# Performance work log

Hardware: AMD Instinct MI355X
Metric: run time of the kernel (lower is better)

## Reference

```python
import jax, jax.numpy as jnp
import numpy as np

B, T, L, H = 512, 512, 64, 512  # batch, time_steps, sequence_len, hidden_dim


def gru_cell(x, h, W_ih, W_hh, b_ih, b_hh):
    # PyTorch GRUCell math. W_ih: [3H, in], W_hh: [3H, H]; gate order (r, z, n).
    gi = x @ W_ih.T + b_ih
    gh = h @ W_hh.T + b_hh
    i_r, i_z, i_n = jnp.split(gi, 3, axis=-1)
    h_r, h_z, h_n = jnp.split(gh, 3, axis=-1)
    r = jax.nn.sigmoid(i_r + h_r)
    z = jax.nn.sigmoid(i_z + h_z)
    n = jnp.tanh(i_n + r * h_n)
    return (1.0 - z) * n + z * h


def setup_inputs() -> dict:
    key = jax.random.key(0)
    ks = jax.random.split(key, 12)
    s = 1.0 / np.sqrt(H)  # PyTorch GRUCell/Linear init scale
    u = lambda k, shape: jax.random.uniform(k, shape, jnp.float32, -s, s)
    return {
        "x": jax.random.normal(ks[0], (B, T + L - 1), jnp.float32),
        "h_1": jnp.zeros((B, H), jnp.float32),
        "h_2": jnp.zeros((B, H), jnp.float32),
        "W_ih1": u(ks[1], (3 * H, T)),
        "W_hh1": u(ks[2], (3 * H, H)),
        "b_ih1": u(ks[3], (3 * H,)),
        "b_hh1": u(ks[4], (3 * H,)),
        "W_ih2": u(ks[5], (3 * H, H)),
        "W_hh2": u(ks[6], (3 * H, H)),
        "b_ih2": u(ks[7], (3 * H,)),
        "b_hh2": u(ks[8], (3 * H,)),
        "W_fc": u(ks[9], (1, H)),
        "b_fc": u(ks[10], (1,)),
    }


def reference(x, h_1, h_2, W_ih1, W_hh1, b_ih1, b_hh1,
              W_ih2, W_hh2, b_ih2, b_hh2, W_fc, b_fc):
    # Sliding windows x[:, t:t+T] for t in [0, L): gather once, scan over steps.
    idx = jnp.arange(L)[:, None] + jnp.arange(T)[None, :]  # [L, T]
    xs = jnp.transpose(x[:, idx], (1, 0, 2))  # [L, B, T]

    def step(carry, x_t):
        h1, h2 = carry
        h1 = gru_cell(x_t, h1, W_ih1, W_hh1, b_ih1, b_hh1)
        h2 = gru_cell(h1, h2, W_ih2, W_hh2, b_ih2, b_hh2)
        y = (h2 @ W_fc.T + b_fc)[:, 0]  # [B]
        return (h1, h2), y

    (h1, h2), ys = jax.lax.scan(step, (h_1, h_2), xs)
    return ys.T, h1, h2  # output_seq [B, L], final hidden states
```

## Files before the change

### kernel.cpp

```cpp
#include <hip/hip_runtime.h>
#include <hip/hip_bf16.h>
#include <math.h>

typedef __attribute__((ext_vector_type(8))) short short8;
typedef __attribute__((ext_vector_type(4))) float f32x4;
typedef unsigned short u16;
typedef unsigned int u32;

__device__ __forceinline__ u16 f2bf(float f) {
  union { float f; u32 u; } x; x.f = f;
  return (u16)((x.u + 0x7fffu + ((x.u >> 16) & 1u)) >> 16);
}
__device__ __forceinline__ float sigm(float v) {
  return __builtin_amdgcn_rcpf(1.0f + __expf(-v));
}
__device__ __forceinline__ float tanh_fast(float v) {
  return 1.0f - 2.0f * __builtin_amdgcn_rcpf(1.0f + __expf(2.0f * v));
}

#define MFMA __builtin_amdgcn_mfma_f32_16x16x32_bf16
#define HS 262144

#define LDG16_BODY(FL)                                        \
    "global_load_dwordx4 %0, %16, off " FL "\n\t"             \
    "global_load_dwordx4 %1, %16, off offset:64 " FL "\n\t"   \
    "global_load_dwordx4 %2, %16, off offset:128 " FL "\n\t"  \
    "global_load_dwordx4 %3, %16, off offset:192 " FL "\n\t"  \
    "global_load_dwordx4 %4, %16, off offset:256 " FL "\n\t"  \
    "global_load_dwordx4 %5, %16, off offset:320 " FL "\n\t"  \
    "global_load_dwordx4 %6, %16, off offset:384 " FL "\n\t"  \
    "global_load_dwordx4 %7, %16, off offset:448 " FL "\n\t"  \
    "global_load_dwordx4 %8, %16, off offset:512 " FL "\n\t"  \
    "global_load_dwordx4 %9, %16, off offset:576 " FL "\n\t"  \
    "global_load_dwordx4 %10, %16, off offset:640 " FL "\n\t" \
    "global_load_dwordx4 %11, %16, off offset:704 " FL "\n\t" \
    "global_load_dwordx4 %12, %16, off offset:768 " FL "\n\t" \
    "global_load_dwordx4 %13, %16, off offset:832 " FL "\n\t" \
    "global_load_dwordx4 %14, %16, off offset:896 " FL "\n\t" \
    "global_load_dwordx4 %15, %16, off offset:960 " FL
#define LDG16_OPS(a, base)                                                     \
    : "=&v"(a[0]), "=&v"(a[1]), "=&v"(a[2]), "=&v"(a[3]), "=&v"(a[4]),         \
      "=&v"(a[5]), "=&v"(a[6]), "=&v"(a[7]), "=&v"(a[8]), "=&v"(a[9]),         \
      "=&v"(a[10]), "=&v"(a[11]), "=&v"(a[12]), "=&v"(a[13]), "=&v"(a[14]),    \
      "=&v"(a[15])                                                             \
    : "v"(base) : "memory"

__device__ __forceinline__ void ldg16nw_sc0(short8 a[16], const u16* base) {
  asm volatile(LDG16_BODY("sc0") LDG16_OPS(a, base));
}
__device__ __forceinline__ void ldg16nw_sc01(short8 a[16], const u16* base) {
  asm volatile(LDG16_BODY("sc0 sc1") LDG16_OPS(a, base));
}
#define VMCNT16() do { asm volatile("s_waitcnt vmcnt(16)" ::: "memory"); \
                       __builtin_amdgcn_sched_barrier(0); } while (0)
#define VMCNT0()  do { asm volatile("s_waitcnt vmcnt(0)"  ::: "memory"); \
                       __builtin_amdgcn_sched_barrier(0); } while (0)

__device__ __forceinline__ void stg_sc01(u32* p, u32 v) {
  asm volatile("global_store_dword %0, %1, off sc0 sc1" :: "v"(p), "v"(v) : "memory");
}
__device__ __forceinline__ u32 ldflag(const u32* p) {
  u32 v;
  asm volatile("global_load_dword %0, %1, off sc0 sc1\n\t"
               "s_waitcnt vmcnt(0)" : "=v"(v) : "v"(p) : "memory");
  return v;
}

__device__ __forceinline__ u32 wait_ge(const u32* flags, u32 target, int lane) {
  const u32* p = flags + (lane & 31);
  u32 v;
  for (;;) {
    v = ldflag(p);
    if (__ballot(v >= target) == ~0ull) break;
    __builtin_amdgcn_s_sleep(1);
  }
  #pragma unroll
  for (int k = 16; k; k >>= 1) {
    u32 o = (u32)__shfl_xor((int)v, k);
    v = v < o ? v : o;
  }
  return v;
}

__global__ __launch_bounds__(256, 1) void gru_fused(
    const float* __restrict__ xin, const float* __restrict__ h1in, const float* __restrict__ h2in,
    const float* __restrict__ Wih1, const float* __restrict__ Whh1,
    const float* __restrict__ bih1, const float* __restrict__ bhh1,
    const float* __restrict__ Wih2, const float* __restrict__ Whh2,
    const float* __restrict__ bih2, const float* __restrict__ bhh2,
    const float* __restrict__ Wfc, const float* __restrict__ bfc,
    float* __restrict__ out, u16* __restrict__ wsb, unsigned* __restrict__ barc)
{
  const int bid   = blockIdx.x;
  const int rb    = bid & 3;
  const int layer = (bid >> 2) & 1;
  const int cbl   = bid >> 3;
  const int n0    = cbl * 16;
  const int wid   = bid >> 2;
  const int tid   = threadIdx.x;
  const int w     = tid >> 6;
  const int lane  = tid & 63;
  const int quad  = lane >> 4;
  const int m16   = lane & 15;

  u16* x0  = wsb;
  u16* x1  = x0 + 512 * 576;
  u16* h1r = x1 + 512 * 576;
  u16* h2r = h1r + 4 * HS;
  u16* h1m = h2r + 4 * HS;

  __shared__ short8 wlds[96 * 64];

  u32* f0    = (u32*)barc + rb * 32;
  u32* f1    = (u32*)barc + 128 + rb * 32;
  unsigned* cinit = barc + 512;

  const float* Wih = layer ? Wih2 : Wih1;
  const float* Whh = layer ? Whh2 : Whh1;
  const float* bih = layer ? bih2 : bih1;
  const float* bhh = layer ? bhh2 : bhh1;

  for (int i = wid * 256 + tid; i < 128 * 575; i += 64 * 256) {
    int r = i / 575, c = i - r * 575;
    int row = rb * 128 + r;
    u16 bv = f2bf(xin[row * 575 + c]);
    x0[row * 576 + c] = bv;
    if (c >= 1) x1[row * 576 + (c - 1)] = bv;
  }
  for (int i = wid * 256 + tid; i < 128 * 512; i += 64 * 256) {
    int r = i >> 9, c = i & 511;
    int row = rb * 128 + r;
    u16 h1v = f2bf(h1in[row * 512 + c]);
    h1r[3 * HS + row * 512 + c] = h1v;
    h2r[3 * HS + row * 512 + c] = f2bf(h2in[row * 512 + c]);
  }
  for (int i = tid; i < 96 * 64; i += 256) {
    int blk = i >> 6, l = i & 63;
    int s, gr;
    if (blk < 64) { s = blk & 31; gr = (blk >> 5) * 512; }
    else          { s = blk - 64; gr = 1024; }
    int n  = n0 + (l & 15);
    int k0 = s * 32 + (l >> 4) * 8;
    short8 pk;
    #pragma unroll
    for (int j = 0; j < 8; ++j) {
      int k = k0 + j;
      float v = (k < 512) ? Wih[(gr + n) * 512 + k] : Whh[(gr + n) * 512 + (k - 512)];
      pk[j] = (short)f2bf(v);
    }
    wlds[blk * 64 + l] = pk;
  }

  float hreg[2][4];
  const float* hin = layer ? h2in : h1in;
  #pragma unroll
  for (int rf = 0; rf < 2; ++rf)
    #pragma unroll
    for (int q = 0; q < 4; ++q)
      hreg[rf][q] = hin[(rb * 128 + (2 * w + rf) * 16 + quad * 4 + q) * 512 + n0 + m16];

  const int nn = n0 + m16;
  const float bias_r  = bih[nn] + bhh[nn];
  const float bias_z  = bih[512 + nn] + bhh[512 + nn];
  const float bias_in = bih[1024 + nn];
  const float bias_hn = bhh[1024 + nn];
  const float wfc  = Wfc[nn];
  const float bfcv = bfc[0];

  __syncthreads();
  if (tid == 0) {
    __builtin_amdgcn_fence(__ATOMIC_RELEASE, "agent");
    __hip_atomic_fetch_add(cinit, 1u, __ATOMIC_RELAXED, __HIP_MEMORY_SCOPE_AGENT);
    while (__hip_atomic_load(cinit, __ATOMIC_RELAXED, __HIP_MEMORY_SCOPE_AGENT) < 256u)
      __builtin_amdgcn_s_sleep(1);
    __builtin_amdgcn_fence(__ATOMIC_ACQUIRE, "agent");
  }
  __syncthreads();

  const int arow0 = rb * 128 + (2 * w) * 16 + m16;
  const int arow1 = arow0 + 16;

  if (layer == 0) {
    u32 c1min = 0;
    for (int u = 0; u < 64; ++u) {
      if (u >= 4 && c1min < (u32)(u - 3)) c1min = wait_ge(f1, (u32)(u - 3), lane);
      f32x4 acc[2][4] = {};
      {
        const int c = u & 1;
        const u16* xc = c ? x1 : x0;
        const u32* pa0 = (const u32*)(xc + (size_t)arow0 * 576 + (u - c) + quad * 8);
        const u32* pa1 = (const u32*)(xc + (size_t)arow1 * 576 + (u - c) + quad * 8);
        #pragma unroll
        for (int s = 0; s < 16; ++s) {
          union { short8 v; u32 u4[4]; } a0, a1;
          #pragma unroll
          for (int j = 0; j < 4; ++j) { a0.u4[j] = pa0[s * 16 + j]; a1.u4[j] = pa1[s * 16 + j]; }
          short8 br = wlds[(s)      * 64 + lane];
          short8 bz = wlds[(32 + s) * 64 + lane];
          short8 bi = wlds[(64 + s) * 64 + lane];
          acc[0][0] = MFMA(a0.v, br, acc[0][0], 0, 0, 0);
          acc[1][0] = MFMA(a1.v, br, acc[1][0], 0, 0, 0);
          acc[0][1] = MFMA(a0.v, bz, acc[0][1], 0, 0, 0);
          acc[1][1] = MFMA(a1.v, bz, acc[1][1], 0, 0, 0);
          acc[0][2] = MFMA(a0.v, bi, acc[0][2], 0, 0, 0);
          acc[1][2] = MFMA(a1.v, bi, acc[1][2], 0, 0, 0);
        }
      }
      if (u > 0) wait_ge(f0, (u32)u, lane); else VMCNT0();
      {
        short8 a0[16], a1[16];
        const u16* hb = h1r + (size_t)((u + 3) & 3) * HS + quad * 8;
        ldg16nw_sc0(a0, hb + (size_t)arow0 * 512);
        ldg16nw_sc0(a1, hb + (size_t)arow1 * 512);
        VMCNT16();
        #pragma unroll
        for (int s = 0; s < 16; ++s) {
          short8 br = wlds[(16 + s) * 64 + lane];
          short8 bz = wlds[(48 + s) * 64 + lane];
          short8 bh = wlds[(80 + s) * 64 + lane];
          acc[0][0] = MFMA(a0[s], br, acc[0][0], 0, 0, 0);
          acc[0][1] = MFMA(a0[s], bz, acc[0][1], 0, 0, 0);
          acc[0][3] = MFMA(a0[s], bh, acc[0][3], 0, 0, 0);
        }
        VMCNT0();
        #pragma unroll
        for (int s = 0; s < 16; ++s) {
          short8 br = wlds[(16 + s) * 64 + lane];
          short8 bz = wlds[(48 + s) * 64 + lane];
          short8 bh = wlds[(80 + s) * 64 + lane];
          acc[1][0] = MFMA(a1[s], br, acc[1][0], 0, 0, 0);
          acc[1][1] = MFMA(a1[s], bz, acc[1][1], 0, 0, 0);
          acc[1][3] = MFMA(a1[s], bh, acc[1][3], 0, 0, 0);
        }
      }
      {
        u32* hw32 = (u32*)(h1r + (size_t)(u & 3) * HS);
        u32* hm   = (u32*)(h1m + (size_t)(u & 3) * HS);
        #pragma unroll
        for (int rf = 0; rf < 2; ++rf)
          #pragma unroll
          for (int q = 0; q < 4; ++q) {
            float rg = sigm(acc[rf][0][q] + bias_r);
            float zg = sigm(acc[rf][1][q] + bias_z);
            float ng = tanh_fast(acc[rf][2][q] + bias_in + rg * (acc[rf][3][q] + bias_hn));
            float hv = (1.0f - zg) * ng + zg * hreg[rf][q];
            hreg[rf][q] = hv;
            int row = rb * 128 + (2 * w + rf) * 16 + quad * 4 + q;
            u16 b = f2bf(hv);
            int pb = __shfl_xor((int)(u32)b, 1);
            if (!(m16 & 1)) {
              u32 pr = (u32)b | ((u32)(u16)pb << 16);
              int pi = (row * 512 + nn) >> 1;
              hw32[pi] = pr;
              stg_sc01(&hm[pi], pr);
            }
          }
      }
      asm volatile("s_waitcnt vmcnt(0)" ::: "memory");
      __syncthreads();
      if (tid == 0) stg_sc01(&f0[cbl], (u32)(u + 1));
    }
  } else {
    for (int v = 0; v < 64; ++v) {
      f32x4 acc[2][4] = {};
      if (v > 0) wait_ge(f1, (u32)v, lane); else VMCNT0();
      {
        short8 a0[16], a1[16];
        const u16* hb = h2r + (size_t)((v + 3) & 3) * HS + quad * 8;
        ldg16nw_sc0(a0, hb + (size_t)arow0 * 512);
        ldg16nw_sc0(a1, hb + (size_t)arow1 * 512);
        VMCNT16();
        #pragma unroll
        for (int s = 0; s < 16; ++s) {
          short8 br = wlds[(16 + s) * 64 + lane];
          short8 bz = wlds[(48 + s) * 64 + lane];
          short8 bh = wlds[(80 + s) * 64 + lane];
          acc[0][0] = MFMA(a0[s], br, acc[0][0], 0, 0, 0);
          acc[0][1] = MFMA(a0[s], bz, acc[0][1], 0, 0, 0);
          acc[0][3] = MFMA(a0[s], bh, acc[0][3], 0, 0, 0);
        }
        VMCNT0();
        #pragma unroll
        for (int s = 0; s < 16; ++s) {
          short8 br = wlds[(16 + s) * 64 + lane];
          short8 bz = wlds[(48 + s) * 64 + lane];
          short8 bh = wlds[(80 + s) * 64 + lane];
          acc[1][0] = MFMA(a1[s], br, acc[1][0], 0, 0, 0);
          acc[1][1] = MFMA(a1[s], bz, acc[1][1], 0, 0, 0);
          acc[1][3] = MFMA(a1[s], bh, acc[1][3], 0, 0, 0);
        }
      }
      wait_ge(f0, (u32)(v + 1), lane);
      {
        short8 a0[16], a1[16];
        const u16* hb = h1m + (size_t)(v & 3) * HS + quad * 8;
        ldg16nw_sc01(a0, hb + (size_t)arow0 * 512);
        ldg16nw_sc01(a1, hb + (size_t)arow1 * 512);
        VMCNT16();
        #pragma unroll
        for (int s = 0; s < 16; ++s) {
          short8 br = wlds[(s)      * 64 + lane];
          short8 bz = wlds[(32 + s) * 64 + lane];
          short8 bi = wlds[(64 + s) * 64 + lane];
          acc[0][0] = MFMA(a0[s], br, acc[0][0], 0, 0, 0);
          acc[0][1] = MFMA(a0[s], bz, acc[0][1], 0, 0, 0);
          acc[0][2] = MFMA(a0[s], bi, acc[0][2], 0, 0, 0);
        }
        VMCNT0();
        #pragma unroll
        for (int s = 0; s < 16; ++s) {
          short8 br = wlds[(s)      * 64 + lane];
          short8 bz = wlds[(32 + s) * 64 + lane];
          short8 bi = wlds[(64 + s) * 64 + lane];
          acc[1][0] = MFMA(a1[s], br, acc[1][0], 0, 0, 0);
          acc[1][1] = MFMA(a1[s], bz, acc[1][1], 0, 0, 0);
          acc[1][2] = MFMA(a1[s], bi, acc[1][2], 0, 0, 0);
        }
      }
      {
        u32* hw32 = (u32*)(h2r + (size_t)(v & 3) * HS);
        #pragma unroll
        for (int rf = 0; rf < 2; ++rf)
          #pragma unroll
          for (int q = 0; q < 4; ++q) {
            float rg = sigm(acc[rf][0][q] + bias_r);
            float zg = sigm(acc[rf][1][q] + bias_z);
            float ng = tanh_fast(acc[rf][2][q] + bias_in + rg * (acc[rf][3][q] + bias_hn));
            float hv = (1.0f - zg) * ng + zg * hreg[rf][q];
            hreg[rf][q] = hv;
            int row = rb * 128 + (2 * w + rf) * 16 + quad * 4 + q;
            u16 b = f2bf(hv);
            int pb = __shfl_xor((int)(u32)b, 1);
            if (!(m16 & 1))
              hw32[(row * 512 + nn) >> 1] = (u32)b | ((u32)(u16)pb << 16);
          }
      }
      asm volatile("s_waitcnt vmcnt(0)" ::: "memory");
      __syncthreads();
      if (tid == 0) stg_sc01(&f1[cbl], (u32)(v + 1));
      #pragma unroll
      for (int rf = 0; rf < 2; ++rf)
        #pragma unroll
        for (int q = 0; q < 4; ++q) {
          float yv = hreg[rf][q] * wfc;
          yv += __shfl_xor(yv, 1);
          yv += __shfl_xor(yv, 2);
          yv += __shfl_xor(yv, 4);
          yv += __shfl_xor(yv, 8);
          if (m16 == 0) {
            int row = rb * 128 + (2 * w + rf) * 16 + quad * 4 + q;
            atomicAdd(&out[row * 64 + v], yv + (n0 == 0 ? bfcv : 0.0f));
          }
        }
    }
  }

  float* hout = out + 32768 + layer * (512 * 512);
  #pragma unroll
  for (int rf = 0; rf < 2; ++rf)
    #pragma unroll
    for (int q = 0; q < 4; ++q) {
      int row = rb * 128 + (2 * w + rf) * 16 + quad * 4 + q;
      hout[row * 512 + nn] = hreg[rf][q];
    }
}

extern "C" void kernel_launch(void* const* d_in, const int* in_sizes, int n_in,
                              void* d_out, int out_size, void* d_ws, size_t ws_size,
                              hipStream_t stream) {
  (void)in_sizes; (void)n_in; (void)out_size; (void)ws_size;
  hipMemsetAsync(d_out, 0, 32768 * sizeof(float), stream);
  hipMemsetAsync(d_ws, 0, 4096, stream);
  unsigned* bar = (unsigned*)d_ws;
  u16* wsb = (u16*)((char*)d_ws + 4096);
  gru_fused<<<256, 256, 0, stream>>>(
      (const float*)d_in[0], (const float*)d_in[1], (const float*)d_in[2],
      (const float*)d_in[3], (const float*)d_in[4], (const float*)d_in[5], (const float*)d_in[6],
      (const float*)d_in[7], (const float*)d_in[8], (const float*)d_in[9], (const float*)d_in[10],
      (const float*)d_in[11], (const float*)d_in[12],
      (float*)d_out, wsb, bar);
}
```

Before: 828.5 us.

## Replace per-block flag arrays with atomic counters and compute FC output from loaded h2

Inter-block synchronization switches from 32-entry per-block flag arrays polled by a whole wavefront to a single atomic counter per row-group, polled by thread 0 and followed by __syncthreads. Layer 1 now waits on both counters at one point instead of two separate waits. The FC projection is no longer done with per-step atomicAdds from every column block. The column-block-0 workgroup instead computes the full dot product from the bf16 h2 tile it already loads, writing the result one step late plus a final epilogue. This removes many global atomics but gives the output bf16-rounded h2 inputs and puts extra ALU work on one block per row group.

```diff
diff --git a/kernel.cpp b/kernel.cpp
--- a/kernel.cpp
+++ b/kernel.cpp
@@ -59,27 +59,36 @@
 __device__ __forceinline__ void stg_sc01(u32* p, u32 v) {
   asm volatile("global_store_dword %0, %1, off sc0 sc1" :: "v"(p), "v"(v) : "memory");
 }
-__device__ __forceinline__ u32 ldflag(const u32* p) {
-  u32 v;
-  asm volatile("global_load_dword %0, %1, off sc0 sc1\n\t"
-               "s_waitcnt vmcnt(0)" : "=v"(v) : "v"(p) : "memory");
-  return v;
-}
-
-__device__ __forceinline__ u32 wait_ge(const u32* flags, u32 target, int lane) {
-  const u32* p = flags + (lane & 31);
-  u32 v;
-  for (;;) {
-    v = ldflag(p);
-    if (__ballot(v >= target) == ~0ull) break;
-    __builtin_amdgcn_s_sleep(1);
-  }
+
+__device__ __forceinline__ void waits_nf(unsigned* a, unsigned ta, unsigned* b, unsigned tb) {
+  if (threadIdx.x == 0) {
+    while (__hip_atomic_load(a, __ATOMIC_RELAXED, __HIP_MEMORY_SCOPE_AGENT) < ta)
+      __builtin_amdgcn_s_sleep(1);
+    while (__hip_atomic_load(b, __ATOMIC_RELAXED, __HIP_MEMORY_SCOPE_AGENT) < tb)
+      __builtin_amdgcn_s_sleep(1);
+  }
+  __syncthreads();
+}
+
+__device__ __forceinline__ float ydot(const short8 a[16], const float* wfcl, int quad) {
+  float y = 0.0f;
   #pragma unroll
-  for (int k = 16; k; k >>= 1) {
-    u32 o = (u32)__shfl_xor((int)v, k);
-    v = v < o ? v : o;
-  }
-  return v;
+  for (int s = 0; s < 16; ++s) {
+    const float4 wa = *(const float4*)&wfcl[32 * s + quad * 8];
+    const float4 wb = *(const float4*)&wfcl[32 * s + quad * 8 + 4];
+    union { short8 v; u32 u4[4]; } aa; aa.v = a[s];
+    #pragma unroll
+    for (int k = 0; k < 4; ++k) {
+      union { u32 u; float f; } lo, hi;
+      lo.u = aa.u4[k] << 16;
+      hi.u = aa.u4[k] & 0xffff0000u;
+      float w0 = (k < 2) ? ((k & 1) ? wa.z : wa.x) : ((k & 1) ? wb.z : wb.x);
+      float w1 = (k < 2) ? ((k & 1) ? wa.w : wa.y) : ((k & 1) ? wb.w : wb.y);
+      y = fmaf(lo.f, w0, y);
+      y = fmaf(hi.f, w1, y);
+    }
+  }
+  return y;
 }
 
 __global__ __launch_bounds__(256, 1) void gru_fused(
@@ -110,9 +119,10 @@
   u16* h1m = h2r + 4 * HS;
 
   __shared__ short8 wlds[96 * 64];
-
-  u32* f0    = (u32*)barc + rb * 32;
-  u32* f1    = (u32*)barc + 128 + rb * 32;
+  __shared__ float wfcl[512];
+
+  unsigned* c0    = barc + rb * 32;
+  unsigned* c1    = barc + 256 + rb * 32;
   unsigned* cinit = barc + 512;
 
   const float* Wih = layer ? Wih2 : Wih1;
@@ -150,6 +160,7 @@
     }
     wlds[blk * 64 + l] = pk;
   }
+  for (int i = tid; i < 512; i += 256) wfcl[i] = Wfc[i];
 
   float hreg[2][4];
   const float* hin = layer ? h2in : h1in;
@@ -164,7 +175,6 @@
   const float bias_z  = bih[512 + nn] + bhh[512 + nn];
   const float bias_in = bih[1024 + nn];
   const float bias_hn = bhh[1024 + nn];
-  const float wfc  = Wfc[nn];
   const float bfcv = bfc[0];
 
   __syncthreads();
@@ -181,9 +191,7 @@
   const int arow1 = arow0 + 16;
 
   if (layer == 0) {
-    u32 c1min = 0;
     for (int u = 0; u < 64; ++u) {
-      if (u >= 4 && c1min < (u32)(u - 3)) c1min = wait_ge(f1, (u32)(u - 3), lane);
       f32x4 acc[2][4] = {};
       {
         const int c = u & 1;
@@ -206,7 +214,7 @@
           acc[1][2] = MFMA(a1.v, bi, acc[1][2], 0, 0, 0);
         }
       }
-      if (u > 0) wait_ge(f0, (u32)u, lane); else VMCNT0();
+      waits_nf(c0, 32u * (unsigned)u, c1, u >= 4 ? 32u * (unsigned)(u - 3) : 0u);
       {
         short8 a0[16], a1[16];
         const u16* hb = h1r + (size_t)((u + 3) & 3) * HS + quad * 8;
@@ -258,12 +266,15 @@
       }
       asm volatile("s_waitcnt vmcnt(0)" ::: "memory");
       __syncthreads();
-      if (tid == 0) stg_sc01(&f0[cbl], (u32)(u + 1));
+      if (tid == 0)
+        __hip_atomic_fetch_add(c0, 1u, __ATOMIC_RELAXED, __HIP_MEMORY_SCOPE_AGENT);
     }
   } else {
+    const bool ywg = (cbl == 0);
     for (int v = 0; v < 64; ++v) {
       f32x4 acc[2][4] = {};
-      if (v > 0) wait_ge(f1, (u32)v, lane); else VMCNT0();
+      waits_nf(c1, 32u * (unsigned)v, c0, 32u * (unsigned)(v + 1));
+      float ya0 = 0.0f, ya1 = 0.0f;
       {
         short8 a0[16], a1[16];
         const u16* hb = h2r + (size_t)((v + 3) & 3) * HS + quad * 8;
@@ -279,6 +290,7 @@
           acc[0][1] = MFMA(a0[s], bz, acc[0][1], 0, 0, 0);
           acc[0][3] = MFMA(a0[s], bh, acc[0][3], 0, 0, 0);
         }
+        if (ywg && v > 0) ya0 = ydot(a0, wfcl, quad);
         VMCNT0();
         #pragma unroll
         for (int s = 0; s < 16; ++s) {
@@ -289,22 +301,22 @@
           acc[1][1] = MFMA(a1[s], bz, acc[1][1], 0, 0, 0);
           acc[1][3] = MFMA(a1[s], bh, acc[1][3], 0, 0, 0);
         }
-      }
-      wait_ge(f0, (u32)(v + 1), lane);
-      {
-        short8 a0[16], a1[16];
+        if (ywg && v > 0) ya1 = ydot(a1, wfcl, quad);
+      }
+      {
+        short8 b0[16], b1[16];
         const u16* hb = h1m + (size_t)(v & 3) * HS + quad * 8;
-        ldg16nw_sc01(a0, hb + (size_t)arow0 * 512);
-        ldg16nw_sc01(a1, hb + (size_t)arow1 * 512);
+        ldg16nw_sc01(b0, hb + (size_t)arow0 * 512);
+        ldg16nw_sc01(b1, hb + (size_t)arow1 * 512);
         VMCNT16();
         #pragma unroll
         for (int s = 0; s < 16; ++s) {
           short8 br = wlds[(s)      * 64 + lane];
           short8 bz = wlds[(32 + s) * 64 + lane];
           short8 bi = wlds[(64 + s) * 64 + lane];
-          acc[0][0] = MFMA(a0[s], br, acc[0][0], 0, 0, 0);
-          acc[0][1] = MFMA(a0[s], bz, acc[0][1], 0, 0, 0);
-          acc[0][2] = MFMA(a0[s], bi, acc[0][2], 0, 0, 0);
+          acc[0][0] = MFMA(b0[s], br, acc[0][0], 0, 0, 0);
+          acc[0][1] = MFMA(b0[s], bz, acc[0][1], 0, 0, 0);
+          acc[0][2] = MFMA(b0[s], bi, acc[0][2], 0, 0, 0);
         }
         VMCNT0();
         #pragma unroll
@@ -312,9 +324,9 @@
           short8 br = wlds[(s)      * 64 + lane];
           short8 bz = wlds[(32 + s) * 64 + lane];
           short8 bi = wlds[(64 + s) * 64 + lane];
-          acc[1][0] = MFMA(a1[s], br, acc[1][0], 0, 0, 0);
-          acc[1][1] = MFMA(a1[s], bz, acc[1][1], 0, 0, 0);
-          acc[1][2] = MFMA(a1[s], bi, acc[1][2], 0, 0, 0);
+          acc[1][0] = MFMA(b1[s], br, acc[1][0], 0, 0, 0);
+          acc[1][1] = MFMA(b1[s], bz, acc[1][1], 0, 0, 0);
+          acc[1][2] = MFMA(b1[s], bi, acc[1][2], 0, 0, 0);
         }
       }
       {
@@ -337,21 +349,33 @@
       }
       asm volatile("s_waitcnt vmcnt(0)" ::: "memory");
       __syncthreads();
-      if (tid == 0) stg_sc01(&f1[cbl], (u32)(v + 1));
-      #pragma unroll
-      for (int rf = 0; rf < 2; ++rf)
-        #pragma unroll
-        for (int q = 0; q < 4; ++q) {
-          float yv = hreg[rf][q] * wfc;
-          yv += __shfl_xor(yv, 1);
-          yv += __shfl_xor(yv, 2);
-          yv += __shfl_xor(yv, 4);
-          yv += __shfl_xor(yv, 8);
-          if (m16 == 0) {
-            int row = rb * 128 + (2 * w + rf) * 16 + quad * 4 + q;
-            atomicAdd(&out[row * 64 + v], yv + (n0 == 0 ? bfcv : 0.0f));
-          }
-        }
+      if (tid == 0)
+        __hip_atomic_fetch_add(c1, 1u, __ATOMIC_RELAXED, __HIP_MEMORY_SCOPE_AGENT);
+      if (ywg && v > 0) {
+        ya0 += __shfl_xor(ya0, 16); ya0 += __shfl_xor(ya0, 32);
+        ya1 += __shfl_xor(ya1, 16); ya1 += __shfl_xor(ya1, 32);
+        if (quad == 0) {
+          out[arow0 * 64 + (v - 1)] = ya0 + bfcv;
+          out[arow1 * 64 + (v - 1)] = ya1 + bfcv;
+        }
+      }
+    }
+    if (ywg) {
+      waits_nf(c1, 32u * 64u, c1, 32u * 64u);
+      short8 a0[16], a1[16];
+      const u16* hb = h2r + (size_t)3 * HS + quad * 8;
+      ldg16nw_sc0(a0, hb + (size_t)arow0 * 512);
+      ldg16nw_sc0(a1, hb + (size_t)arow1 * 512);
+      VMCNT16();
+      float ya0 = ydot(a0, wfcl, quad);
+      VMCNT0();
+      float ya1 = ydot(a1, wfcl, quad);
+      ya0 += __shfl_xor(ya0, 16); ya0 += __shfl_xor(ya0, 32);
+      ya1 += __shfl_xor(ya1, 16); ya1 += __shfl_xor(ya1, 32);
+      if (quad == 0) {
+        out[arow0 * 64 + 63] = ya0 + bfcv;
+        out[arow1 * 64 + 63] = ya1 + bfcv;
+      }
     }
   }
 
```

Result: faster. 801.9 us (-3.2%).
